# Kernel tuning notes

Hardware: AMD Instinct MI355X
Metric: run time of the kernel (lower is better)

The kernel has to match this reference:

```python
import jax, jax.numpy as jnp
import numpy as np

B, S, D, H = 8, 2048, 256, 256


def setup_inputs() -> dict:
    key = jax.random.key(0)
    ks = jax.random.split(key, 7)
    s_ih = 1.0 / np.sqrt(D)
    s_hh = 1.0 / np.sqrt(H)
    return {
        "x": jax.random.normal(ks[0], (B, S, D), dtype=jnp.float32),
        "Wih_f": jax.random.uniform(ks[1], (4 * H, D), jnp.float32, -s_ih, s_ih),
        "bih_f": jax.random.uniform(ks[2], (4 * H,), jnp.float32, -s_ih, s_ih),
        "Whh_f": jax.random.uniform(ks[3], (4 * H, H), jnp.float32, -s_hh, s_hh),
        "Wih_b": jax.random.uniform(ks[4], (4 * H, D), jnp.float32, -s_ih, s_ih),
        "bih_b": jax.random.uniform(ks[5], (4 * H,), jnp.float32, -s_ih, s_ih),
        "Whh_b": jax.random.uniform(ks[6], (4 * H, H), jnp.float32, -s_hh, s_hh),
    }


def _lstm_dir(x, Wih, bih, Whh, reverse):
    # Precompute input projection for all timesteps in one GEMM: [B,S,4H]
    b, s, _ = x.shape
    h_dim = Whh.shape[1]
    x_proj = jnp.einsum("bsd,gd->bsg", x, Wih) + bih

    def step(carry, xt):  # xt: [B,4H]
        h, c = carry
        gates = xt + h @ Whh.T
        i, f, g, o = jnp.split(gates, 4, axis=-1)
        i = jax.nn.sigmoid(i)
        f = jax.nn.sigmoid(f)
        o = jax.nn.sigmoid(o)
        g = jnp.tanh(g)
        c = f * c + i * g
        h = o * jnp.tanh(c)
        return (h, c), h

    init = (jnp.zeros((b, h_dim), x.dtype), jnp.zeros((b, h_dim), x.dtype))
    # scan over time; reverse=True processes t=S-1..0 and stacks outputs in
    # original time order, matching the torch backward loop with insert(0, .)
    _, hs = jax.lax.scan(step, init, jnp.swapaxes(x_proj, 0, 1), reverse=reverse)
    return jnp.swapaxes(hs, 0, 1)  # [B,S,H]


def reference(x, Wih_f, bih_f, Whh_f, Wih_b, bih_b, Whh_b):
    fwd = _lstm_dir(x, Wih_f, bih_f, Whh_f, reverse=False)
    bwd = _lstm_dir(x, Wih_b, bih_b, Whh_b, reverse=True)
    return jnp.concatenate([fwd, bwd], axis=-1)  # [B,S,2H]
```

## Files before the change

### kernel.cpp

```cpp
#include <hip/hip_runtime.h>
#include <hip/hip_bf16.h>
#include <stdint.h>

#define SQ   2048
#define NB   8
#define G4   1024
#define NROW 16384

typedef float f32x4 __attribute__((ext_vector_type(4)));
typedef short bf16x8 __attribute__((ext_vector_type(8)));
typedef uint32_t u32;
typedef unsigned long long u64;

__device__ __forceinline__ f32x4 mfma16(bf16x8 a, bf16x8 b, f32x4 c) {
  return __builtin_amdgcn_mfma_f32_16x16x32_bf16(a, b, c, 0, 0, 0);
}
__device__ __forceinline__ u32 pk_bf16(float lo, float hi) {
  u32 r;
  asm("v_cvt_pk_bf16_f32 %0, %1, %2" : "=v"(r) : "v"(lo), "v"(hi));
  return r;
}
__device__ __forceinline__ float bf_lo(u32 u){ union{u32 a; float f;} x; x.a = u << 16;        return x.f; }
__device__ __forceinline__ float bf_hi(u32 u){ union{u32 a; float f;} x; x.a = u & 0xffff0000u; return x.f; }

__device__ __forceinline__ float sigm(float x)   { return 1.0f / (1.0f + __expf(-x)); }
__device__ __forceinline__ float tanh_f(float x) { return 1.0f - 2.0f / (__expf(2.0f * x) + 1.0f); }

__global__ __launch_bounds__(256) void xproj_gemm(
    const float* __restrict__ x,
    const float* __restrict__ WihF, const float* __restrict__ bihF,
    const float* __restrict__ WihB, const float* __restrict__ bihB,
    uint16_t* __restrict__ xp)
{
  const int dir = blockIdx.z;
  const float* Wih = dir ? WihB : WihF;
  const float* bih = dir ? bihB : bihF;
  char* xpd = (char*)xp + (size_t)dir * ((size_t)NROW * G4 * 2);

  const int g0 = blockIdx.y * 128;
  const int m0 = blockIdx.x * 128;

  __shared__ union {
    struct { short A[128 * 72]; short B[128 * 72]; } s;
    short T[128 * 136];
  } u;
  __shared__ float biasS[128];

  const int tid  = threadIdx.x;
  const int lane = tid & 63;
  const int w    = tid >> 6;
  const int wg   = w >> 1;
  const int wm   = w & 1;
  const int l15  = lane & 15;
  const int l4   = lane >> 4;

  if (tid < 128) biasS[tid] = bih[g0 + tid];

  f32x4 acc[4][4] = {};

  const int r_st = tid >> 1;
  const int half = tid & 1;
  const int mrow_st = m0 + r_st;
  const int xb = mrow_st & 7;
  const int xt = mrow_st >> 3;
  const float* xrow = x + ((size_t)xb * SQ + xt) * 256;
  const float* wrow = Wih + (size_t)(g0 + r_st) * 256;

  for (int s = 0; s < 4; ++s) {
    const int k0 = s * 64;
    __syncthreads();
    {
      const float* srcA = wrow + k0 + half * 32;
      const float* srcB = xrow + k0 + half * 32;
      short* dstA = u.s.A + r_st * 72 + half * 32;
      short* dstB = u.s.B + r_st * 72 + half * 32;
      #pragma unroll
      for (int j = 0; j < 4; ++j) {
        f32x4 a0 = *(const f32x4*)(srcA + j * 8);
        f32x4 a1 = *(const f32x4*)(srcA + j * 8 + 4);
        uint4 pa = { pk_bf16(a0.x, a0.y), pk_bf16(a0.z, a0.w),
                     pk_bf16(a1.x, a1.y), pk_bf16(a1.z, a1.w) };
        *(uint4*)(dstA + j * 8) = pa;
        f32x4 b0 = *(const f32x4*)(srcB + j * 8);
        f32x4 b1 = *(const f32x4*)(srcB + j * 8 + 4);
        uint4 pb = { pk_bf16(b0.x, b0.y), pk_bf16(b0.z, b0.w),
                     pk_bf16(b1.x, b1.y), pk_bf16(b1.z, b1.w) };
        *(uint4*)(dstB + j * 8) = pb;
      }
    }
    __syncthreads();
    #pragma unroll
    for (int kt = 0; kt < 2; ++kt) {
      bf16x8 aF[4], bF[4];
      #pragma unroll
      for (int i = 0; i < 4; ++i) {
        const int ar = wg * 64 + i * 16 + l15;
        const int br = wm * 64 + i * 16 + l15;
        aF[i] = *(const bf16x8*)(u.s.A + ar * 72 + kt * 32 + l4 * 8);
        bF[i] = *(const bf16x8*)(u.s.B + br * 72 + kt * 32 + l4 * 8);
      }
      #pragma unroll
      for (int i = 0; i < 4; ++i)
        #pragma unroll
        for (int j = 0; j < 4; ++j)
          acc[i][j] = mfma16(aF[i], bF[j], acc[i][j]);
    }
  }

  __syncthreads();
  #pragma unroll
  for (int i = 0; i < 4; ++i) {
    const f32x4 bv = *(const f32x4*)(biasS + wg * 64 + i * 16 + l4 * 4);
    #pragma unroll
    for (int j = 0; j < 4; ++j) {
      f32x4 v = acc[i][j];
      v.x += bv.x; v.y += bv.y; v.z += bv.z; v.w += bv.w;
      const int mrow = wm * 64 + j * 16 + l15;
      const int gcol = wg * 64 + i * 16 + l4 * 4;
      uint2 p; p.x = pk_bf16(v.x, v.y); p.y = pk_bf16(v.z, v.w);
      *(uint2*)(u.T + mrow * 136 + gcol) = p;
    }
  }
  __syncthreads();
  {
    const char* trow = (const char*)(u.T + r_st * 136);
    char* orow = xpd + (size_t)(m0 + r_st) * 2048 + g0 * 2;
    #pragma unroll
    for (int j = 0; j < 8; ++j) {
      const int local = half * 128 + j * 16;
      uint4 v = *(const uint4*)(trow + local);
      *(uint4*)(orow + local) = v;
    }
  }
}

template<int HALF>
__device__ __forceinline__ void lstm_body(
    const float* __restrict__ Whh, const uint16_t* __restrict__ xpd,
    float* __restrict__ out, u64* ex_me, u64* ex_pt, int dir,
    uint16_t (*hT)[8][136], uint16_t (*hP)[8][136])
{
  const int tid  = threadIdx.x;
  const int lane = tid & 63;
  const int w    = tid >> 6;
  const int l15  = lane & 15;
  const int l4   = lane >> 4;
  const int bcl  = lane & 7;
  const int qsel = (lane >> 3) & 1;

  bf16x8 W[4][8];
  #pragma unroll
  for (int g = 0; g < 4; ++g) {
    const int row = g * 256 + HALF * 128 + w * 16 + l15;
    const float* src = Whh + (size_t)row * 256 + l4 * 8;
    #pragma unroll
    for (int kt = 0; kt < 8; ++kt) {
      f32x4 v0 = *(const f32x4*)(src + kt * 32);
      f32x4 v1 = *(const f32x4*)(src + kt * 32 + 4);
      union { bf16x8 v; u32 u[4]; } pk;
      pk.u[0] = pk_bf16(v0.x, v0.y); pk.u[1] = pk_bf16(v0.z, v0.w);
      pk.u[2] = pk_bf16(v1.x, v1.y); pk.u[3] = pk_bf16(v1.z, v1.w);
      W[g][kt] = pk.v;
    }
  }

  const int d0   = w * 16 + l4 * 4 + qsel * 2;
  const int word = bcl * 64 + (d0 >> 1);
  float c0 = 0.0f, c1 = 0.0f;

  u32 xq[4];
  {
    const int tt0 = dir ? SQ - 1 : 0;
    const uint16_t* xr = xpd + (size_t)(tt0 * 8 + bcl) * 1024 + HALF * 128 + d0;
    #pragma unroll
    for (int g = 0; g < 4; ++g) xq[g] = *(const u32*)(xr + g * 256);
  }

  u64 pw = 0;

  #pragma unroll 1
  for (int t = 0; t < SQ; ++t) {
    const int tt = dir ? (SQ - 1 - t) : t;

    if (t > 0) {
      const u32 want = (u32)t;
      u64* pa = ex_pt + (size_t)((t - 1) & 1) * 512 + tid;
      while ((u32)pw != want) {
        __builtin_amdgcn_s_sleep(1);
        pw = __hip_atomic_load(pa, __ATOMIC_RELAXED, __HIP_MEMORY_SCOPE_AGENT);
      }
      *(u32*)&hP[(t - 1) & 1][w][lane * 2] = (u32)(pw >> 32);
    }
    asm volatile("s_waitcnt lgkmcnt(0)" ::: "memory");
    __builtin_amdgcn_s_barrier();

    f32x4 acc[4] = {};
    if (t > 0) {
      #pragma unroll
      for (int ko = 0; ko < 4; ++ko) {
        const bf16x8 bO = *(const bf16x8*)&hT[t & 1][bcl][ko * 32 + l4 * 8];
        #pragma unroll
        for (int g = 0; g < 4; ++g) acc[g] = mfma16(W[g][HALF * 4 + ko], bO, acc[g]);
        const bf16x8 bP = *(const bf16x8*)&hP[(t - 1) & 1][bcl][ko * 32 + l4 * 8];
        #pragma unroll
        for (int g = 0; g < 4; ++g) acc[g] = mfma16(W[g][(1 - HALF) * 4 + ko], bP, acc[g]);
      }
    }

    float P0[4], P1[4];
    #pragma unroll
    for (int g = 0; g < 4; ++g) {
      P0[g] = (qsel ? acc[g].z : acc[g].x) + bf_lo(xq[g]);
      P1[g] = (qsel ? acc[g].w : acc[g].y) + bf_hi(xq[g]);
    }
    const float i0 = sigm(P0[0]), f0 = sigm(P0[1]), g0v = tanh_f(P0[2]), o0 = sigm(P0[3]);
    const float i1 = sigm(P1[0]), f1 = sigm(P1[1]), g1v = tanh_f(P1[2]), o1 = sigm(P1[3]);
    c0 = f0 * c0 + i0 * g0v;
    c1 = f1 * c1 + i1 * g1v;
    const float h0 = o0 * tanh_f(c0);
    const float h1 = o1 * tanh_f(c1);

    *(float2*)(out + ((size_t)bcl * SQ + tt) * 512 + dir * 256 + HALF * 128 + d0) =
        make_float2(h0, h1);
    const u32 h01 = pk_bf16(h0, h1);
    __hip_atomic_store(ex_me + (size_t)(t & 1) * 512 + word,
                       ((u64)h01 << 32) | (u64)(u32)(t + 1),
                       __ATOMIC_RELAXED, __HIP_MEMORY_SCOPE_AGENT);
    *(u32*)&hT[(t + 1) & 1][bcl][d0] = h01;

    {
      const int tn = (t + 1 < SQ) ? t + 1 : SQ - 1;
      const int ttn = dir ? (SQ - 1 - tn) : tn;
      const uint16_t* xr = xpd + (size_t)(ttn * 8 + bcl) * 1024 + HALF * 128 + d0;
      #pragma unroll
      for (int g = 0; g < 4; ++g) xq[g] = *(const u32*)(xr + g * 256);
    }
    pw = __hip_atomic_load(ex_pt + (size_t)(t & 1) * 512 + tid,
                           __ATOMIC_RELAXED, __HIP_MEMORY_SCOPE_AGENT);
  }
}

__global__ __launch_bounds__(512, 2) void lstm_rec(
    const float* __restrict__ WhhF, const float* __restrict__ WhhB,
    const uint16_t* __restrict__ xp, float* __restrict__ out, u64* exch)
{
  __shared__ uint16_t hT[2][8][136];
  __shared__ uint16_t hP[2][8][136];

  const int bid  = blockIdx.x;
  const int dir  = bid & 7;
  const int half = bid >> 3;
  if (dir > 1) return;

  const float* Whh = dir ? WhhB : WhhF;
  const uint16_t* xpd = xp + (size_t)dir * NROW * G4;
  u64* eme = exch + (size_t)(dir * 2 + half) * 1024;
  u64* ept = exch + (size_t)(dir * 2 + (1 - half)) * 1024;

  if (half == 0) lstm_body<0>(Whh, xpd, out, eme, ept, dir, hT, hP);
  else           lstm_body<1>(Whh, xpd, out, eme, ept, dir, hT, hP);
}

extern "C" void kernel_launch(void* const* d_in, const int* in_sizes, int n_in,
                              void* d_out, int out_size, void* d_ws, size_t ws_size,
                              hipStream_t stream) {
  const float* x    = (const float*)d_in[0];
  const float* WihF = (const float*)d_in[1];
  const float* bihF = (const float*)d_in[2];
  const float* WhhF = (const float*)d_in[3];
  const float* WihB = (const float*)d_in[4];
  const float* bihB = (const float*)d_in[5];
  const float* WhhB = (const float*)d_in[6];
  float* out = (float*)d_out;

  const size_t XPB = (size_t)2 * NROW * G4 * 2;
  const size_t EXB = (size_t)4096 * sizeof(u64);
  if (ws_size < XPB + EXB) return;
  uint16_t* xpw = (uint16_t*)d_ws;
  u64* exch = (u64*)((char*)d_ws + XPB);

  hipMemsetAsync(exch, 0, EXB, stream);
  xproj_gemm<<<dim3(128, 8, 2), dim3(256), 0, stream>>>(x, WihF, bihF, WihB, bihB, xpw);
  lstm_rec<<<dim3(16), dim3(512), 0, stream>>>(WhhF, WhhB, xpw, out, exch);
}
```

Baseline: 5.972 ms.

## Add dual-path cross-block exchange with fast sc0 polling and adaptive fallback

Each h value is now published to two exchange buffers. One is written and polled with raw global loads and stores marked sc0 and with no sleep. The other uses the original agent-scope atomics and serves as a fallback after a few failed tries, and polling switches to it for good once the fast path keeps timing out. The next step's x-projection prefetch now happens after the barrier, and the weight registers are pinned. The aim is lower latency on the per-step inter-block handoff, at the cost of a second store per step and reliance on sc0 coherence behaviour.

```diff
diff --git a/kernel.cpp b/kernel.cpp
--- a/kernel.cpp
+++ b/kernel.cpp
@@ -25,6 +25,18 @@
 
 __device__ __forceinline__ float sigm(float x)   { return 1.0f / (1.0f + __expf(-x)); }
 __device__ __forceinline__ float tanh_f(float x) { return 1.0f - 2.0f / (__expf(2.0f * x) + 1.0f); }
+
+#define PIN(x) asm volatile("" : "+v"(x))
+
+__device__ __forceinline__ u64 ld_fast(const u64* p) {
+  u64 v;
+  asm volatile("global_load_dwordx2 %0, %1, off sc0\n\ts_waitcnt vmcnt(0)"
+               : "=v"(v) : "v"(p) : "memory");
+  return v;
+}
+__device__ __forceinline__ void st_fast(u64* p, u64 v) {
+  asm volatile("global_store_dwordx2 %0, %1, off sc0" :: "v"(p), "v"(v) : "memory");
+}
 
 __global__ __launch_bounds__(256) void xproj_gemm(
     const float* __restrict__ x,
@@ -137,7 +149,8 @@
 template<int HALF>
 __device__ __forceinline__ void lstm_body(
     const float* __restrict__ Whh, const uint16_t* __restrict__ xpd,
-    float* __restrict__ out, u64* ex_me, u64* ex_pt, int dir,
+    float* __restrict__ out,
+    u64* exf_me, u64* exs_me, const u64* exf_pt, const u64* exs_pt, int dir,
     uint16_t (*hT)[8][136], uint16_t (*hP)[8][136])
 {
   const int tid  = threadIdx.x;
@@ -161,6 +174,7 @@
       pk.u[0] = pk_bf16(v0.x, v0.y); pk.u[1] = pk_bf16(v0.z, v0.w);
       pk.u[2] = pk_bf16(v1.x, v1.y); pk.u[3] = pk_bf16(v1.z, v1.w);
       W[g][kt] = pk.v;
+      PIN(W[g][kt]);
     }
   }
 
@@ -168,7 +182,7 @@
   const int word = bcl * 64 + (d0 >> 1);
   float c0 = 0.0f, c1 = 0.0f;
 
-  u32 xq[4];
+  u32 xq[4], xqn[4];
   {
     const int tt0 = dir ? SQ - 1 : 0;
     const uint16_t* xr = xpd + (size_t)(tt0 * 8 + bcl) * 1024 + HALF * 128 + d0;
@@ -176,7 +190,8 @@
     for (int g = 0; g < 4; ++g) xq[g] = *(const u32*)(xr + g * 256);
   }
 
-  u64 pw = 0;
+  int thr = 8;
+  int slowWins = 0;
 
   #pragma unroll 1
   for (int t = 0; t < SQ; ++t) {
@@ -184,15 +199,31 @@
 
     if (t > 0) {
       const u32 want = (u32)t;
-      u64* pa = ex_pt + (size_t)((t - 1) & 1) * 512 + tid;
-      while ((u32)pw != want) {
-        __builtin_amdgcn_s_sleep(1);
-        pw = __hip_atomic_load(pa, __ATOMIC_RELAXED, __HIP_MEMORY_SCOPE_AGENT);
+      const size_t off = (size_t)((t - 1) & 1) * 512 + tid;
+      u64 pw;
+      int tries = 0;
+      for (;;) {
+        if (tries < thr)
+          pw = ld_fast(exf_pt + off);
+        else
+          pw = __hip_atomic_load(exs_pt + off, __ATOMIC_RELAXED,
+                                 __HIP_MEMORY_SCOPE_AGENT);
+        if ((u32)pw == want) break;
+        ++tries;
       }
+      if (thr > 0 && tries >= thr) { if (++slowWins >= 4) thr = 0; }
       *(u32*)&hP[(t - 1) & 1][w][lane * 2] = (u32)(pw >> 32);
     }
     asm volatile("s_waitcnt lgkmcnt(0)" ::: "memory");
     __builtin_amdgcn_s_barrier();
+
+    {
+      const int tn = (t + 1 < SQ) ? t + 1 : SQ - 1;
+      const int ttn = dir ? (SQ - 1 - tn) : tn;
+      const uint16_t* xr = xpd + (size_t)(ttn * 8 + bcl) * 1024 + HALF * 128 + d0;
+      #pragma unroll
+      for (int g = 0; g < 4; ++g) xqn[g] = *(const u32*)(xr + g * 256);
+    }
 
     f32x4 acc[4] = {};
     if (t > 0) {
@@ -220,29 +251,24 @@
     const float h0 = o0 * tanh_f(c0);
     const float h1 = o1 * tanh_f(c1);
 
+    const u32 h01 = pk_bf16(h0, h1);
+    const u64 pub = ((u64)h01 << 32) | (u64)(u32)(t + 1);
+    st_fast(exf_me + (size_t)(t & 1) * 512 + word, pub);
+    __hip_atomic_store(exs_me + (size_t)(t & 1) * 512 + word, pub,
+                       __ATOMIC_RELAXED, __HIP_MEMORY_SCOPE_AGENT);
+    *(u32*)&hT[(t + 1) & 1][bcl][d0] = h01;
     *(float2*)(out + ((size_t)bcl * SQ + tt) * 512 + dir * 256 + HALF * 128 + d0) =
         make_float2(h0, h1);
-    const u32 h01 = pk_bf16(h0, h1);
-    __hip_atomic_store(ex_me + (size_t)(t & 1) * 512 + word,
-                       ((u64)h01 << 32) | (u64)(u32)(t + 1),
-                       __ATOMIC_RELAXED, __HIP_MEMORY_SCOPE_AGENT);
-    *(u32*)&hT[(t + 1) & 1][bcl][d0] = h01;
-
-    {
-      const int tn = (t + 1 < SQ) ? t + 1 : SQ - 1;
-      const int ttn = dir ? (SQ - 1 - tn) : tn;
-      const uint16_t* xr = xpd + (size_t)(ttn * 8 + bcl) * 1024 + HALF * 128 + d0;
-      #pragma unroll
-      for (int g = 0; g < 4; ++g) xq[g] = *(const u32*)(xr + g * 256);
-    }
-    pw = __hip_atomic_load(ex_pt + (size_t)(t & 1) * 512 + tid,
-                           __ATOMIC_RELAXED, __HIP_MEMORY_SCOPE_AGENT);
+
+    #pragma unroll
+    for (int g = 0; g < 4; ++g) xq[g] = xqn[g];
   }
 }
 
 __global__ __launch_bounds__(512, 2) void lstm_rec(
     const float* __restrict__ WhhF, const float* __restrict__ WhhB,
-    const uint16_t* __restrict__ xp, float* __restrict__ out, u64* exch)
+    const uint16_t* __restrict__ xp, float* __restrict__ out,
+    u64* exs, u64* exf)
 {
   __shared__ uint16_t hT[2][8][136];
   __shared__ uint16_t hP[2][8][136];
@@ -254,11 +280,13 @@
 
   const float* Whh = dir ? WhhB : WhhF;
   const uint16_t* xpd = xp + (size_t)dir * NROW * G4;
-  u64* eme = exch + (size_t)(dir * 2 + half) * 1024;
-  u64* ept = exch + (size_t)(dir * 2 + (1 - half)) * 1024;
-
-  if (half == 0) lstm_body<0>(Whh, xpd, out, eme, ept, dir, hT, hP);
-  else           lstm_body<1>(Whh, xpd, out, eme, ept, dir, hT, hP);
+  const size_t me = (size_t)(dir * 2 + half) * 1024;
+  const size_t pt = (size_t)(dir * 2 + (1 - half)) * 1024;
+
+  if (half == 0)
+    lstm_body<0>(Whh, xpd, out, exf + me, exs + me, exf + pt, exs + pt, dir, hT, hP);
+  else
+    lstm_body<1>(Whh, xpd, out, exf + me, exs + me, exf + pt, exs + pt, dir, hT, hP);
 }
 
 extern "C" void kernel_launch(void* const* d_in, const int* in_sizes, int n_in,
@@ -275,11 +303,12 @@
 
   const size_t XPB = (size_t)2 * NROW * G4 * 2;
   const size_t EXB = (size_t)4096 * sizeof(u64);
-  if (ws_size < XPB + EXB) return;
+  if (ws_size < XPB + 2 * EXB) return;
   uint16_t* xpw = (uint16_t*)d_ws;
-  u64* exch = (u64*)((char*)d_ws + XPB);
-
-  hipMemsetAsync(exch, 0, EXB, stream);
+  u64* exs = (u64*)((char*)d_ws + XPB);
+  u64* exf = (u64*)((char*)d_ws + XPB + EXB);
+
+  hipMemsetAsync(exs, 0, 2 * EXB, stream);
   xproj_gemm<<<dim3(128, 8, 2), dim3(256), 0, stream>>>(x, WihF, bihF, WihB, bihB, xpw);
-  lstm_rec<<<dim3(16), dim3(512), 0, stream>>>(WhhF, WhhB, xpw, out, exch);
-}
+  lstm_rec<<<dim3(16), dim3(512), 0, stream>>>(WhhF, WhhB, xpw, out, exs, exf);
+}
```

New measurement: 6.597 ms. 10.5% more time.
